# Performance work log

Hardware: AMD Instinct MI355X
Metric: run time of the kernel (lower is better)

Reference implementation:

```python
import jax, jax.numpy as jnp
import numpy as np
from functools import partial

STRIDES = (8, 16, 32, 64)
SCORE_T = 0.25
NMS_T = 0.45
MAX_DET = 300
PRE_NMS_K = 512  # fixed candidate budget replacing data-dependent torch.where


def _decode_level(cls, reg, kpt, stride):
    # cls: (C,H,W), reg: (4,H,W), kpt: (10,H,W) for one image, one level
    score = jax.nn.sigmoid(cls).max(axis=0)               # (H,W) max over classes
    H, W = score.shape
    ys, xs = jnp.meshgrid(jnp.arange(H, dtype=cls.dtype),
                          jnp.arange(W, dtype=cls.dtype), indexing='ij')
    cx = (xs + 0.5) * stride
    cy = (ys + 0.5) * stride
    cxd = cx + reg[0] * stride
    cyd = cy + reg[1] * stride
    w = jnp.exp(reg[2]) * stride
    h = jnp.exp(reg[3]) * stride
    boxes = jnp.stack([cxd - w / 2, cyd - h / 2, cxd + w / 2, cyd + h / 2], axis=-1)
    boxes = boxes.reshape(-1, 4)                           # (HW,4) xyxy
    kx = cx[None] + kpt[0::2] * stride                     # (5,H,W)
    ky = cy[None] + kpt[1::2] * stride                     # (5,H,W)
    kpts = jnp.stack([kx, ky], axis=-1)                    # (5,H,W,2)
    kpts = kpts.transpose(1, 2, 0, 3).reshape(-1, 5, 2)    # (HW,5,2)
    return boxes, score.reshape(-1), kpts


def _pairwise_iou(b):
    # b: (K,4) xyxy -> (K,K) IoU, same convention as torchvision.ops.nms
    x1 = jnp.maximum(b[:, None, 0], b[None, :, 0])
    y1 = jnp.maximum(b[:, None, 1], b[None, :, 1])
    x2 = jnp.minimum(b[:, None, 2], b[None, :, 2])
    y2 = jnp.minimum(b[:, None, 3], b[None, :, 3])
    inter = jnp.clip(x2 - x1, 0) * jnp.clip(y2 - y1, 0)
    area = (b[:, 2] - b[:, 0]) * (b[:, 3] - b[:, 1])
    union = area[:, None] + area[None, :] - inter
    return inter / jnp.maximum(union, 1e-9)


def _nms_keep(boxes, valid):
    # boxes sorted by descending score; greedy NMS via suppression sweep
    K = boxes.shape[0]
    ious = _pairwise_iou(boxes)
    idx = jnp.arange(K)

    def body(i, keep):
        sup = keep[i] & (ious[i] > NMS_T) & (idx > i)
        return keep & ~sup

    return jax.lax.fori_loop(0, K, body, valid)


def _per_image(boxes, scores, kpts):
    # boxes (N,4), scores (N,), kpts (N,5,2) concatenated over all levels
    masked = jnp.where(scores > SCORE_T, scores, 0.0)      # score-threshold mask
    top_s, top_i = jax.lax.top_k(masked, PRE_NMS_K)        # sorted descending
    b = boxes[top_i]                                       # (K,4)
    k = kpts[top_i]                                        # (K,5,2)
    valid = top_s > SCORE_T
    keep = _nms_keep(b, valid)
    # compact kept detections (in score order) into first MAX_DET slots
    rank = jnp.cumsum(keep) - 1
    slot = jnp.where(keep & (rank < MAX_DET), rank, MAX_DET)
    feat = jnp.concatenate([b, top_s[:, None], k.reshape(PRE_NMS_K, 10)], axis=1)  # (K,15)
    buf = jnp.zeros((MAX_DET + 1, 15), feat.dtype).at[slot].set(feat)
    return buf[:MAX_DET]                                   # (MAX_DET, 15): [x1,y1,x2,y2,score,kpts*10]


def setup_inputs() -> dict:
    key = jax.random.key(0)
    B = 16
    sizes = (256, 128, 64, 32)
    keys = jax.random.split(key, 12)
    inp = {}
    for li, s in enumerate(sizes):
        inp[f'cls{li}'] = jax.random.normal(keys[li], (B, 1, s, s), jnp.float32)
        inp[f'reg{li}'] = jax.random.normal(keys[4 + li], (B, 4, s, s), jnp.float32)
        inp[f'kpt{li}'] = jax.random.normal(keys[8 + li], (B, 10, s, s), jnp.float32)
    return inp


def reference(cls0, cls1, cls2, cls3, reg0, reg1, reg2, reg3, kpt0, kpt1, kpt2, kpt3):
    clss = (cls0, cls1, cls2, cls3)
    regs = (reg0, reg1, reg2, reg3)
    kpts = (kpt0, kpt1, kpt2, kpt3)
    bs, ss, ks = [], [], []
    for c, r, k, stride in zip(clss, regs, kpts, STRIDES):
        dec = jax.vmap(partial(_decode_level, stride=stride))
        b, s, kp = dec(c, r, k)
        bs.append(b); ss.append(s); ks.append(kp)
    boxes = jnp.concatenate(bs, axis=1)    # (B, N, 4)
    scores = jnp.concatenate(ss, axis=1)   # (B, N)
    keypts = jnp.concatenate(ks, axis=1)   # (B, N, 5, 2)
    return jax.vmap(_per_image)(boxes, scores, keypts)  # (B, MAX_DET, 15)
```

## Files before the change

### kernel.cpp

```cpp
#include <hip/hip_runtime.h>
#include <stdint.h>

#define CAP_   2048
#define KSEL   512
#define MAXDET 300
#define NIMG   16
#define SCORE_T 0.25f
#define NMS_T   0.45f
#define HBINS  72
#define SLICES 8
#define PERSLICE 2720
#define RCH    128


__device__ __forceinline__ float sigmoidf_(float x) {
  return 1.0f / (1.0f + expf(-x));
}

__device__ __forceinline__ float4 load_cls4_(const float* c0, const float* c1,
                                             const float* c2, const float* c3,
                                             int b, int g) {
  if (g < 16384) return ((const float4*)(c0 + (size_t)b * 65536))[g];
  if (g < 20480) return ((const float4*)(c1 + (size_t)b * 16384))[g - 16384];
  if (g < 21504) return ((const float4*)(c2 + (size_t)b * 4096))[g - 20480];
  return ((const float4*)(c3 + (size_t)b * 1024))[g - 21504];
}

__global__ __launch_bounds__(1024)
void k_scan(const float* __restrict__ c0, const float* __restrict__ c1,
            const float* __restrict__ c2, const float* __restrict__ c3,
            uint32_t* __restrict__ histS, uint32_t* __restrict__ cnt) {
  const int b = blockIdx.x >> 3;
  const int slice = blockIdx.x & 7;
  const int tid = threadIdx.x;
  const int wave = tid >> 6;

  __shared__ uint32_t lh[16][HBINS];
  for (int i = tid; i < 16 * HBINS; i += 1024) ((uint32_t*)lh)[i] = 0;
  __syncthreads();

  for (int it = 0; it < 3; ++it) {
    int lg = it * 1024 + tid;
    if (lg < PERSLICE) {
      int g = slice * PERSLICE + lg;
      float4 v = load_cls4_(c0, c1, c2, c3, b, g);
      float sv[4] = {v.x, v.y, v.z, v.w};
#pragma unroll
      for (int e = 0; e < 4; ++e) {
        float s = sigmoidf_(sv[e]);
        if (s > SCORE_T) {
          uint32_t bin = (__float_as_uint(s) >> 18) - 4000u;
          if (bin > 64u) bin = 64u;
          atomicAdd(&lh[wave][bin], 1u);
        }
      }
    }
  }
  __syncthreads();

  if (tid < HBINS) {
    uint32_t s = 0;
#pragma unroll
    for (int w = 0; w < 16; ++w) s += lh[w][tid];
    histS[blockIdx.x * HBINS + tid] = s;
  }
  if (blockIdx.x == 0 && tid < NIMG) cnt[tid] = 0;
}

__global__ __launch_bounds__(1024)
void k_compact(const float* __restrict__ c0, const float* __restrict__ c1,
               const float* __restrict__ c2, const float* __restrict__ c3,
               const uint32_t* __restrict__ histS,
               uint32_t* __restrict__ cnt, uint64_t* __restrict__ keys) {
  const int b = blockIdx.x >> 3;
  const int slice = blockIdx.x & 7;
  const int tid = threadIdx.x;

  __shared__ uint64_t lk[CAP_];
  __shared__ uint32_t lcnt;
  __shared__ uint32_t gbase;
  __shared__ uint32_t s_tot[HBINS];
  __shared__ uint32_t s_thrv;

  if (tid == 0) lcnt = 0;
  if (tid < HBINS) {
    uint32_t s = 0;
#pragma unroll
    for (int sl = 0; sl < SLICES; ++sl)
      s += histS[(b * SLICES + sl) * HBINS + tid];
    s_tot[tid] = s;
  }
  __syncthreads();

  if (tid < 64) {
    uint32_t x = s_tot[tid];
    if (tid == 63) x += s_tot[64];
    for (int off = 1; off < 64; off <<= 1) {
      uint32_t v = __shfl_down(x, off);
      if (tid + off < 64) x += v;
    }
    uint32_t nxt = __shfl_down(x, 1);
    if (tid == 63) nxt = 0;
    bool cross = (x >= KSEL) && (nxt < KSEL);
    unsigned long long m = __ballot(cross);
    if (tid == 0) {
      int bucket = m ? (__ffsll(m) - 1) : 0;
      s_thrv = ((uint32_t)(4000 + bucket)) << 18;
    }
  }
  __syncthreads();

  const uint32_t tb = s_thrv;

  for (int it = 0; it < 3; ++it) {
    int lg = it * 1024 + tid;
    if (lg < PERSLICE) {
      int g = slice * PERSLICE + lg;
      float4 v = load_cls4_(c0, c1, c2, c3, b, g);
      float sv[4] = {v.x, v.y, v.z, v.w};
#pragma unroll
      for (int e = 0; e < 4; ++e) {
        float s = sigmoidf_(sv[e]);
        if (s > SCORE_T) {
          uint32_t bits = __float_as_uint(s);
          if (bits >= tb) {
            uint32_t n = (uint32_t)(4 * g + e);
            uint32_t p = atomicAdd(&lcnt, 1u);
            if (p < CAP_)
              lk[p] = ((uint64_t)bits << 32) | (0xFFFFFFFFu - n);
          }
        }
      }
    }
  }
  __syncthreads();

  if (tid == 0) {
    uint32_t c = lcnt > CAP_ ? CAP_ : lcnt;
    gbase = atomicAdd(&cnt[b], c);
  }
  __syncthreads();

  uint32_t c = lcnt > CAP_ ? CAP_ : lcnt;
  for (uint32_t i = tid; i < c; i += 1024) {
    uint32_t pos = gbase + i;
    if (pos < CAP_) keys[(size_t)b * CAP_ + pos] = lk[i];
  }
}

__global__ __launch_bounds__(1024)
void k_rank(const uint64_t* __restrict__ keys, const uint32_t* __restrict__ cnt,
            const float* __restrict__ r0p, const float* __restrict__ r1p,
            const float* __restrict__ r2p, const float* __restrict__ r3p,
            uint64_t* __restrict__ skeys, float* __restrict__ bxs) {
  const int b = blockIdx.x >> 4;
  const int chunk = blockIdx.x & 15;
  const int t = threadIdx.x;

  __shared__ __align__(16) uint64_t lkey[CAP_];
  __shared__ uint32_t part[RCH][9];

  int c = (int)cnt[b];
  if (c > CAP_) c = CAP_;
  for (int i = t; i < CAP_; i += 1024)
    lkey[i] = (i < c) ? keys[(size_t)b * CAP_ + i] : 0ull;
  __syncthreads();

  const int ci   = t & (RCH - 1);
  const int cand = chunk * RCH + ci;
  const int seg  = t >> 7;
  const uint64_t mykey = lkey[cand];
  uint32_t pc = 0;
  const ulonglong2* lk2 = (const ulonglong2*)lkey;
#pragma unroll 4
  for (int j2 = seg * 128; j2 < seg * 128 + 128; ++j2) {
    ulonglong2 kk = lk2[j2];
    pc += (kk.x > mykey) ? 1u : 0u;
    pc += (kk.y > mykey) ? 1u : 0u;
  }
  part[ci][seg] = pc;
  __syncthreads();

  if (t < RCH) {
    int rank = 0;
#pragma unroll
    for (int s = 0; s < 8; ++s) rank += part[t][s];
    if (cand < c && rank < KSEL) {
      uint64_t key = mykey;
      float sc = __uint_as_float((uint32_t)(key >> 32));
      float x1 = 0.f, y1 = 0.f, x2 = 0.f, y2 = 0.f;
      if (sc > SCORE_T) {
        int n = (int)(0xFFFFFFFFu - (uint32_t)key);
        const float* rp; int local, Nl, logW; float st;
        if (n < 65536)      { rp = r0p + (size_t)b * 4 * 65536; local = n;          Nl = 65536; logW = 8; st = 8.f;  }
        else if (n < 81920) { rp = r1p + (size_t)b * 4 * 16384; local = n - 65536;  Nl = 16384; logW = 7; st = 16.f; }
        else if (n < 86016) { rp = r2p + (size_t)b * 4 * 4096;  local = n - 81920;  Nl = 4096;  logW = 6; st = 32.f; }
        else                { rp = r3p + (size_t)b * 4 * 1024;  local = n - 86016;  Nl = 1024;  logW = 5; st = 64.f; }
        int y = local >> logW, x = local & ((1 << logW) - 1);
        float cx = ((float)x + 0.5f) * st;
        float cy = ((float)y + 0.5f) * st;
        float rv0 = rp[local];
        float rv1 = rp[Nl + local];
        float rv2 = rp[2 * Nl + local];
        float rv3 = rp[3 * Nl + local];
        float cxd = cx + rv0 * st;
        float cyd = cy + rv1 * st;
        float w = expf(rv2) * st;
        float h = expf(rv3) * st;
        x1 = cxd - w * 0.5f; y1 = cyd - h * 0.5f;
        x2 = cxd + w * 0.5f; y2 = cyd + h * 0.5f;
      }
      skeys[(size_t)b * KSEL + rank] = key;
      float* base = bxs + (size_t)b * 5 * KSEL;
      base[rank]            = x1;
      base[KSEL + rank]     = y1;
      base[2 * KSEL + rank] = x2;
      base[3 * KSEL + rank] = y2;
      base[4 * KSEL + rank] = (x2 - x1) * (y2 - y1);
    }
  }

  if (chunk == 0) {
    int slot = t - 512;
    if (slot >= 0 && slot < KSEL && slot >= c) {
      skeys[(size_t)b * KSEL + slot] = 0ull;
      float* base = bxs + (size_t)b * 5 * KSEL;
      base[slot]            = 0.f;
      base[KSEL + slot]     = 0.f;
      base[2 * KSEL + slot] = 0.f;
      base[3 * KSEL + slot] = 0.f;
      base[4 * KSEL + slot] = 0.f;
    }
  }
}

__global__ __launch_bounds__(512)
void k_sup(const float* __restrict__ bxs, uint64_t* __restrict__ supT) {
  const int b = blockIdx.x >> 3, chunk = blockIdx.x & 7;
  const int tid = threadIdx.x, wave = tid >> 6, lane = tid & 63;

  __shared__ float sx1[KSEL], sy1[KSEL], sx2[KSEL], sy2[KSEL], sar[KSEL];
  const float* base = bxs + (size_t)b * 5 * KSEL;
  sx1[tid] = base[tid];
  sy1[tid] = base[KSEL + tid];
  sx2[tid] = base[2 * KSEL + tid];
  sy2[tid] = base[3 * KSEL + tid];
  sar[tid] = base[4 * KSEL + tid];
  __syncthreads();

  for (int task = wave; task < 512; task += 8) {
    int i = (chunk << 6) + (task >> 3);
    int w = task & 7;
    int jj = (w << 6) | lane;
    float xx1 = fmaxf(sx1[i], sx1[jj]);
    float yy1 = fmaxf(sy1[i], sy1[jj]);
    float xx2 = fminf(sx2[i], sx2[jj]);
    float yy2 = fminf(sy2[i], sy2[jj]);
    float inter = fmaxf(xx2 - xx1, 0.f) * fmaxf(yy2 - yy1, 0.f);
    float uni = sar[i] + sar[jj] - inter;
    float iou = inter / fmaxf(uni, 1e-9f);
    bool pred = (jj < i) && (iou > NMS_T);
    unsigned long long word = __ballot(pred);
    if (lane == 0) supT[((size_t)b * KSEL + i) * 8 + w] = word;
  }
}

__global__ __launch_bounds__(512)
void k_sweep(const uint64_t* __restrict__ skeys, const float* __restrict__ bxs,
             const uint64_t* __restrict__ supT,
             const float* __restrict__ p0, const float* __restrict__ p1,
             const float* __restrict__ p2, const float* __restrict__ p3,
             float* __restrict__ out) {
  const int b = blockIdx.x;
  const int t = threadIdx.x;
  const int wave = t >> 6, lane = t & 63;

  __shared__ uint64_t keepW[8];
  __shared__ int s_changed;

  const uint64_t* rp_ = supT + ((size_t)b * KSEL + t) * 8;
  uint64_t row0 = rp_[0], row1 = rp_[1], row2 = rp_[2], row3 = rp_[3],
           row4 = rp_[4], row5 = rp_[5], row6 = rp_[6], row7 = rp_[7];

  uint64_t key = skeys[(size_t)b * KSEL + t];
  float sc = __uint_as_float((uint32_t)(key >> 32));
  bool valid = sc > SCORE_T;
  {
    unsigned long long v = __ballot(valid);
    if (lane == 0) keepW[wave] = v;
  }
  __syncthreads();

  for (int pass = 0; pass < KSEL; ++pass) {
    uint64_t k0 = keepW[0], k1 = keepW[1], k2 = keepW[2], k3 = keepW[3],
             k4 = keepW[4], k5 = keepW[5], k6 = keepW[6], k7 = keepW[7];
    __syncthreads();
    if (t == 0) s_changed = 0;
    bool supd = (((k0 & row0) | (k1 & row1) | (k2 & row2) | (k3 & row3) |
                  (k4 & row4) | (k5 & row5) | (k6 & row6) | (k7 & row7)) != 0ull);
    bool nk = valid && !supd;
    unsigned long long wv = __ballot(nk);
    uint64_t oldw;
    switch (wave) {
      case 0: oldw = k0; break; case 1: oldw = k1; break;
      case 2: oldw = k2; break; case 3: oldw = k3; break;
      case 4: oldw = k4; break; case 5: oldw = k5; break;
      case 6: oldw = k6; break; default: oldw = k7; break;
    }
    __syncthreads();
    if (lane == 0) {
      keepW[wave] = wv;
      if (wv != oldw) s_changed = 1;
    }
    __syncthreads();
    if (!s_changed) break;
  }

  uint64_t f0 = keepW[0], f1 = keepW[1], f2 = keepW[2], f3 = keepW[3],
           f4 = keepW[4], f5 = keepW[5], f6 = keepW[6], f7 = keepW[7];
  int ntot = __popcll(f0) + __popcll(f1) + __popcll(f2) + __popcll(f3) +
             __popcll(f4) + __popcll(f5) + __popcll(f6) + __popcll(f7);
  int nwrite = ntot > MAXDET ? MAXDET : ntot;

  {
    int w = wave, bit = lane;
    uint64_t myw;
    switch (w) {
      case 0: myw = f0; break; case 1: myw = f1; break;
      case 2: myw = f2; break; case 3: myw = f3; break;
      case 4: myw = f4; break; case 5: myw = f5; break;
      case 6: myw = f6; break; default: myw = f7; break;
    }
    bool kept = (myw >> bit) & 1ull;
    if (kept) {
      uint64_t pref[8] = {f0, f1, f2, f3, f4, f5, f6, f7};
      int r = 0;
#pragma unroll
      for (int u = 0; u < 8; ++u) {
        if (u < w) r += __popcll(pref[u]);
        else if (u == w) r += __popcll(pref[u] & ((bit == 0) ? 0ull : ((1ull << bit) - 1ull)));
      }
      if (r < MAXDET) {
        int n = (int)(0xFFFFFFFFu - (uint32_t)key);
        const float* kp; int local, Nl, logW; float st;
        if (n < 65536)      { kp = p0 + (size_t)b * 10 * 65536; local = n;          Nl = 65536; logW = 8; st = 8.f;  }
        else if (n < 81920) { kp = p1 + (size_t)b * 10 * 16384; local = n - 65536;  Nl = 16384; logW = 7; st = 16.f; }
        else if (n < 86016) { kp = p2 + (size_t)b * 10 * 4096;  local = n - 81920;  Nl = 4096;  logW = 6; st = 32.f; }
        else                { kp = p3 + (size_t)b * 10 * 1024;  local = n - 86016;  Nl = 1024;  logW = 5; st = 64.f; }
        int y = local >> logW, x = local & ((1 << logW) - 1);
        float cx = ((float)x + 0.5f) * st;
        float cy = ((float)y + 0.5f) * st;
        const float* bb = bxs + (size_t)b * 5 * KSEL;
        float* o = out + ((size_t)b * MAXDET + r) * 15;
        o[0] = bb[t];
        o[1] = bb[KSEL + t];
        o[2] = bb[2 * KSEL + t];
        o[3] = bb[3 * KSEL + t];
        o[4] = sc;
#pragma unroll
        for (int q = 0; q < 5; ++q) {
          float kx = cx + kp[(2 * q) * Nl + local] * st;
          float ky = cy + kp[(2 * q + 1) * Nl + local] * st;
          o[5 + 2 * q] = kx;
          o[6 + 2 * q] = ky;
        }
      }
    }
  }

  if (t < MAXDET && t >= nwrite) {
    float* o = out + ((size_t)b * MAXDET + t) * 15;
#pragma unroll
    for (int e = 0; e < 15; ++e) o[e] = 0.f;
  }
}

extern "C" void kernel_launch(void* const* d_in, const int* in_sizes, int n_in,
                              void* d_out, int out_size, void* d_ws, size_t ws_size,
                              hipStream_t stream) {
  const float* cls0 = (const float*)d_in[0];
  const float* reg0 = (const float*)d_in[1];
  const float* kpt0 = (const float*)d_in[2];
  const float* cls1 = (const float*)d_in[3];
  const float* reg1 = (const float*)d_in[4];
  const float* kpt1 = (const float*)d_in[5];
  const float* cls2 = (const float*)d_in[6];
  const float* reg2 = (const float*)d_in[7];
  const float* kpt2 = (const float*)d_in[8];
  const float* cls3 = (const float*)d_in[9];
  const float* reg3 = (const float*)d_in[10];
  const float* kpt3 = (const float*)d_in[11];
  float* out = (float*)d_out;

  uint8_t* ws = (uint8_t*)d_ws;
  uint32_t* histS = (uint32_t*)ws;
  float*    bxs   = (float*)   ws;
  uint32_t* cnt   = (uint32_t*)(ws + 163840);
  uint64_t* skeys = (uint64_t*)(ws + 163904);
  uint64_t* keys  = (uint64_t*)(ws + 229440);
  uint64_t* supT  = (uint64_t*)(ws + 229440);

  k_scan<<<NIMG * SLICES, 1024, 0, stream>>>(cls0, cls1, cls2, cls3, histS, cnt);
  k_compact<<<NIMG * SLICES, 1024, 0, stream>>>(cls0, cls1, cls2, cls3, histS, cnt, keys);
  k_rank<<<NIMG * 16, 1024, 0, stream>>>(keys, cnt, reg0, reg1, reg2, reg3, skeys, bxs);
  k_sup<<<NIMG * 8, 512, 0, stream>>>(bxs, supT);
  k_sweep<<<NIMG, 512, 0, stream>>>(skeys, bxs, supT,
                                    kpt0, kpt1, kpt2, kpt3, out);
}
```

Baseline: 44.42 us.

## Restructure NMS sweep into per-wave staged fixpoint and trim rank work

The sweep kernel previously iterated a block-wide fixpoint with several __syncthreads per pass. It now resolves suppression one 64-candidate chunk at a time: the owning wave iterates its intra-chunk fixpoint with ballots only, publishes its keep word, and later waves fold it into an external-suppressed flag, so there are 8 block barriers in total. The rank kernel also moves to 64-candidate chunks across twice as many blocks, exits early for chunks past the candidate count, and bounds the comparison loop to the live key count. The trade-off is that the chunks are now resolved serially, wave by wave, and each rank block still loads the full key array into shared memory.

```diff
diff --git a/kernel.cpp b/kernel.cpp
--- a/kernel.cpp
+++ b/kernel.cpp
@@ -10,7 +10,7 @@
 #define HBINS  72
 #define SLICES 8
 #define PERSLICE 2720
-#define RCH    128
+#define RCH    64
 
 
 __device__ __forceinline__ float sigmoidf_(float x) {
@@ -153,27 +153,32 @@
             const float* __restrict__ r0p, const float* __restrict__ r1p,
             const float* __restrict__ r2p, const float* __restrict__ r3p,
             uint64_t* __restrict__ skeys, float* __restrict__ bxs) {
-  const int b = blockIdx.x >> 4;
-  const int chunk = blockIdx.x & 15;
+  const int b = blockIdx.x >> 5;
+  const int chunk = blockIdx.x & 31;
   const int t = threadIdx.x;
 
   __shared__ __align__(16) uint64_t lkey[CAP_];
-  __shared__ uint32_t part[RCH][9];
+  __shared__ uint32_t part[RCH][17];
 
   int c = (int)cnt[b];
   if (c > CAP_) c = CAP_;
+  if (chunk != 0 && chunk * RCH >= c) return;
+
   for (int i = t; i < CAP_; i += 1024)
     lkey[i] = (i < c) ? keys[(size_t)b * CAP_ + i] : 0ull;
   __syncthreads();
 
   const int ci   = t & (RCH - 1);
+  const int seg  = t >> 6;
   const int cand = chunk * RCH + ci;
-  const int seg  = t >> 7;
   const uint64_t mykey = lkey[cand];
+  const int hi2 = (c + 1) >> 1;
+  int j2beg = seg * 64;
+  int j2end = j2beg + 64; if (j2end > hi2) j2end = hi2;
   uint32_t pc = 0;
   const ulonglong2* lk2 = (const ulonglong2*)lkey;
 #pragma unroll 4
-  for (int j2 = seg * 128; j2 < seg * 128 + 128; ++j2) {
+  for (int j2 = j2beg; j2 < j2end; ++j2) {
     ulonglong2 kk = lk2[j2];
     pc += (kk.x > mykey) ? 1u : 0u;
     pc += (kk.y > mykey) ? 1u : 0u;
@@ -184,9 +189,10 @@
   if (t < RCH) {
     int rank = 0;
 #pragma unroll
-    for (int s = 0; s < 8; ++s) rank += part[t][s];
-    if (cand < c && rank < KSEL) {
-      uint64_t key = mykey;
+    for (int s = 0; s < 16; ++s) rank += part[t][s];
+    int cand0 = chunk * RCH + t;
+    if (cand0 < c && rank < KSEL) {
+      uint64_t key = lkey[cand0];
       float sc = __uint_as_float((uint32_t)(key >> 32));
       float x1 = 0.f, y1 = 0.f, x2 = 0.f, y2 = 0.f;
       if (sc > SCORE_T) {
@@ -275,8 +281,7 @@
   const int t = threadIdx.x;
   const int wave = t >> 6, lane = t & 63;
 
-  __shared__ uint64_t keepW[8];
-  __shared__ int s_changed;
+  __shared__ uint64_t keepS[8];
 
   const uint64_t* rp_ = supT + ((size_t)b * KSEL + t) * 8;
   uint64_t row0 = rp_[0], row1 = rp_[1], row2 = rp_[2], row3 = rp_[3],
@@ -285,39 +290,46 @@
   uint64_t key = skeys[(size_t)b * KSEL + t];
   float sc = __uint_as_float((uint32_t)(key >> 32));
   bool valid = sc > SCORE_T;
-  {
-    unsigned long long v = __ballot(valid);
-    if (lane == 0) keepW[wave] = v;
-  }
-  __syncthreads();
-
-  for (int pass = 0; pass < KSEL; ++pass) {
-    uint64_t k0 = keepW[0], k1 = keepW[1], k2 = keepW[2], k3 = keepW[3],
-             k4 = keepW[4], k5 = keepW[5], k6 = keepW[6], k7 = keepW[7];
-    __syncthreads();
-    if (t == 0) s_changed = 0;
-    bool supd = (((k0 & row0) | (k1 & row1) | (k2 & row2) | (k3 & row3) |
-                  (k4 & row4) | (k5 & row5) | (k6 & row6) | (k7 & row7)) != 0ull);
-    bool nk = valid && !supd;
-    unsigned long long wv = __ballot(nk);
-    uint64_t oldw;
-    switch (wave) {
-      case 0: oldw = k0; break; case 1: oldw = k1; break;
-      case 2: oldw = k2; break; case 3: oldw = k3; break;
-      case 4: oldw = k4; break; case 5: oldw = k5; break;
-      case 6: oldw = k6; break; default: oldw = k7; break;
-    }
-    __syncthreads();
-    if (lane == 0) {
-      keepW[wave] = wv;
-      if (wv != oldw) s_changed = 1;
-    }
-    __syncthreads();
-    if (!s_changed) break;
-  }
-
-  uint64_t f0 = keepW[0], f1 = keepW[1], f2 = keepW[2], f3 = keepW[3],
-           f4 = keepW[4], f5 = keepW[5], f6 = keepW[6], f7 = keepW[7];
+
+  uint64_t myintra;
+  switch (wave) {
+    case 0: myintra = row0; break; case 1: myintra = row1; break;
+    case 2: myintra = row2; break; case 3: myintra = row3; break;
+    case 4: myintra = row4; break; case 5: myintra = row5; break;
+    case 6: myintra = row6; break; default: myintra = row7; break;
+  }
+
+  bool extsup = false;
+
+#define STAGE(CH, ROWCH)                                                   \
+  {                                                                        \
+    if (wave == CH) {                                                      \
+      uint64_t a = __ballot(valid && !extsup);                             \
+      while (true) {                                                       \
+        bool nk = valid && !extsup && ((myintra & a) == 0ull);             \
+        uint64_t a2 = __ballot(nk);                                        \
+        if (a2 == a) break;                                                \
+        a = a2;                                                            \
+      }                                                                    \
+      if (lane == 0) keepS[CH] = a;                                        \
+    }                                                                      \
+    __syncthreads();                                                       \
+    { uint64_t kch = keepS[CH];                                            \
+      extsup = extsup || ((ROWCH & kch) != 0ull); }                        \
+  }
+
+  STAGE(0, row0)
+  STAGE(1, row1)
+  STAGE(2, row2)
+  STAGE(3, row3)
+  STAGE(4, row4)
+  STAGE(5, row5)
+  STAGE(6, row6)
+  STAGE(7, row7)
+#undef STAGE
+
+  uint64_t f0 = keepS[0], f1 = keepS[1], f2 = keepS[2], f3 = keepS[3],
+           f4 = keepS[4], f5 = keepS[5], f6 = keepS[6], f7 = keepS[7];
   int ntot = __popcll(f0) + __popcll(f1) + __popcll(f2) + __popcll(f3) +
              __popcll(f4) + __popcll(f5) + __popcll(f6) + __popcll(f7);
   int nwrite = ntot > MAXDET ? MAXDET : ntot;
@@ -402,7 +414,7 @@
 
   k_scan<<<NIMG * SLICES, 1024, 0, stream>>>(cls0, cls1, cls2, cls3, histS, cnt);
   k_compact<<<NIMG * SLICES, 1024, 0, stream>>>(cls0, cls1, cls2, cls3, histS, cnt, keys);
-  k_rank<<<NIMG * 16, 1024, 0, stream>>>(keys, cnt, reg0, reg1, reg2, reg3, skeys, bxs);
+  k_rank<<<NIMG * 32, 1024, 0, stream>>>(keys, cnt, reg0, reg1, reg2, reg3, skeys, bxs);
   k_sup<<<NIMG * 8, 512, 0, stream>>>(bxs, supT);
   k_sweep<<<NIMG, 512, 0, stream>>>(skeys, bxs, supT,
                                     kpt0, kpt1, kpt2, kpt3, out);
```

New measurement: 42.13 us. 1.05x faster.
